# Performance work log

Measured on AMD Instinct MI355X. Metric: run time of the kernel, lower is better.

The kernel has to match this reference:

```python
import jax, jax.numpy as jnp
import numpy as np

HOPS = 3

def setup_inputs() -> dict:
    key = jax.random.key(0)
    ks = jax.random.split(key, 8)
    B, M, S, C, V, D = 16, 200, 32, 2048, 32000, 128
    stories = jax.random.randint(ks[0], (B, M, S), 0, V)
    query = jax.random.randint(ks[1], (B, S), 0, V)
    E = jax.random.randint(ks[2], (B, C, S), 0, V)
    candidates = jax.random.randint(ks[3], (C, S), 0, V)
    # nn.Embedding / nn.Linear weights init: normal(0, 0.1); embedding row 0 zeroed (pad)
    embed_A = (jax.random.normal(ks[4], (V, D), jnp.float32) * 0.1).at[0].set(0.0)
    embed_W = (jax.random.normal(ks[5], (V, D), jnp.float32) * 0.1).at[0].set(0.0)
    H_w = jax.random.normal(ks[6], (D, D), jnp.float32) * 0.1
    H_b = jnp.zeros((D,), jnp.float32)
    return {"stories": stories, "query": query, "E": E, "candidates": candidates,
            "embed_A": embed_A, "embed_W": embed_W, "H_w": H_w, "H_b": H_b}

def reference(stories, query, E, candidates, embed_A, embed_W, H_w, H_b):
    # query embedding, summed over sentence words -> [B, D]
    u = embed_A[query].sum(axis=1)
    # story sentence embeddings summed over words -> [B, M, D]
    # (original recomputes this every hop; value is identical, compute once)
    m = embed_A[stories].sum(axis=2)
    for _ in range(HOPS):
        attn = jax.nn.softmax(jnp.einsum('bmd,bd->bm', m, u), axis=-1)  # [B, M]
        o = jnp.einsum('bm,bmd->bd', attn, m)                            # [B, D]
        u = u @ H_w.T + H_b + o                                          # linear_H(u) + o
    # candidate embeddings: shared candidates table + per-batch mask E, summed over words
    # (embed_W[cand] + embed_W[E]).sum over sentence == sum(embed_W[cand]) + sum(embed_W[E])
    cand_sum = embed_W[candidates].sum(axis=1)[None, :, :] + embed_W[E].sum(axis=2)  # [B, C, D]
    logits = jnp.einsum('bd,bcd->bc', u, cand_sum)  # [B, C]
    return logits
```

## Files before the change

kernel.cpp:

```cpp
#include <hip/hip_runtime.h>

#define B_ 16
#define M_ 200
#define S_ 32
#define C_ 2048
#define V_ 32000
#define D_ 128
#define HOPS_ 3

__global__ void k_embed(const int* __restrict__ stories, const int* __restrict__ query,
                        const float* __restrict__ embA,
                        float* __restrict__ m, float* __restrict__ u0) {
    int lane = threadIdx.x & 31;
    int sent = (blockIdx.x * 256 + threadIdx.x) >> 5;
    if (sent >= B_ * M_ + B_) return;
    const int* idx;
    float* dst;
    if (sent < B_ * M_) { idx = stories + sent * S_; dst = m + sent * D_; }
    else { int b = sent - B_ * M_; idx = query + b * S_; dst = u0 + b * D_; }
    float4 acc = {0.f, 0.f, 0.f, 0.f};
#pragma unroll 8
    for (int s = 0; s < S_; ++s) {
        const float4* row = (const float4*)(embA + (size_t)idx[s] * D_);
        float4 a = row[lane];
        acc.x += a.x; acc.y += a.y; acc.z += a.z; acc.w += a.w;
    }
    ((float4*)dst)[lane] = acc;
}

__global__ void __launch_bounds__(1024) k_hops(
        const float* __restrict__ m, const float* __restrict__ u0,
        const float* __restrict__ Hw, const float* __restrict__ Hb,
        float* __restrict__ uF) {
    const int b = blockIdx.x;
    const int t = threadIdx.x;
    const int lane = t & 63;
    const int wave = t >> 6;

    __shared__ float sm[M_][D_];
    __shared__ float su[D_];
    __shared__ float sattn[M_];
    __shared__ float sred[16 * D_];
    __shared__ float smx, ssum;

    {
        const float4* src = (const float4*)(m + (size_t)b * M_ * D_);
        float4* dst = (float4*)sm;
        for (int j = t; j < M_ * D_ / 4; j += 1024) dst[j] = src[j];
    }
    if (t < D_) su[t] = u0[b * D_ + t];
    __syncthreads();

    for (int hop = 0; hop < HOPS_; ++hop) {
        float2 uu = ((const float2*)su)[lane];
        for (int i = wave; i < M_; i += 16) {
            float2 mv = ((const float2*)sm[i])[lane];
            float p = mv.x * uu.x + mv.y * uu.y;
#pragma unroll
            for (int o = 32; o; o >>= 1) p += __shfl_xor(p, o);
            if (lane == 0) sattn[i] = p;
        }
        __syncthreads();
        if (wave == 0) {
            float mx = -3.0e38f;
            for (int i = lane; i < M_; i += 64) mx = fmaxf(mx, sattn[i]);
#pragma unroll
            for (int o = 32; o; o >>= 1) mx = fmaxf(mx, __shfl_xor(mx, o));
            float sm_ = 0.f;
            for (int i = lane; i < M_; i += 64) sm_ += expf(sattn[i] - mx);
#pragma unroll
            for (int o = 32; o; o >>= 1) sm_ += __shfl_xor(sm_, o);
            if (lane == 0) { smx = mx; ssum = sm_; }
        }
        __syncthreads();
        if (t < M_) sattn[t] = expf(sattn[t] - smx) * (1.f / ssum);
        __syncthreads();
        float2 oacc = {0.f, 0.f};
        for (int i = wave; i < M_; i += 16) {
            float a = sattn[i];
            float2 mv = ((const float2*)sm[i])[lane];
            oacc.x += a * mv.x; oacc.y += a * mv.y;
        }
        ((float2*)sred)[wave * 64 + lane] = oacc;
        __syncthreads();
        int d  = t >> 3;
        int k8 = t & 7;
        float tot = sred[k8 * D_ + d] + sred[(k8 + 8) * D_ + d];
        for (int k = k8; k < D_; k += 8) tot += Hw[d * D_ + k] * su[k];
#pragma unroll
        for (int o = 1; o < 8; o <<= 1) tot += __shfl_xor(tot, o);
        float un = Hb[d] + tot;
        __syncthreads();
        if (k8 == 0) su[d] = un;
        __syncthreads();
    }
    if (t < D_) uF[b * D_ + t] = su[t];
}

__global__ void __launch_bounds__(256) k_pv(
        const float* __restrict__ uF, const float* __restrict__ embW,
        float* __restrict__ P) {
    const int t = threadIdx.x;
    const int gtid = blockIdx.x * 256 + t;
    const int v = gtid >> 2;
    const int q = t & 3;

    __shared__ float4 su4[16 * 36];
    {
#pragma unroll
        for (int it = 0; it < 2; ++it) {
            int f = t + it * 256;
            int b = f >> 5, k = f & 31;
            su4[b * 36 + (k >> 3) * 9 + (k & 7)] = ((const float4*)uF)[f];
        }
    }
    __syncthreads();

    const float4* w = (const float4*)(embW + (size_t)v * D_) + q * 8;
    float acc[16];
#pragma unroll
    for (int b = 0; b < 16; ++b) acc[b] = 0.f;
#pragma unroll
    for (int j = 0; j < 8; ++j) {
        float4 a = w[j];
#pragma unroll
        for (int b = 0; b < 16; ++b) {
            float4 x = su4[b * 36 + q * 9 + j];
            acc[b] += a.x * x.x + a.y * x.y + a.z * x.z + a.w * x.w;
        }
    }
#pragma unroll
    for (int b = 0; b < 16; ++b) {
        acc[b] += __shfl_xor(acc[b], 1);
        acc[b] += __shfl_xor(acc[b], 2);
    }
    float4 o;
    o.x = acc[q * 4 + 0]; o.y = acc[q * 4 + 1];
    o.z = acc[q * 4 + 2]; o.w = acc[q * 4 + 3];
    ((float4*)(P + (size_t)v * B_))[q] = o;
}

__global__ void k_logits(const int* __restrict__ cand, const int* __restrict__ E,
                         const float* __restrict__ P, float* __restrict__ out) {
    int g4 = blockIdx.x * 256 + threadIdx.x;
    int q = g4 & 3;
    int g = g4 >> 2;
    int c = g & (C_ - 1);
    int b = g >> 11;
    const int4* cs = (const int4*)(cand + c * S_ + q * 8);
    const int4* es = (const int4*)(E + (size_t)g * S_ + q * 8);
    float acc = 0.f;
#pragma unroll
    for (int j = 0; j < 2; ++j) {
        int4 wv = cs[j];
        acc += P[wv.x * B_ + b] + P[wv.y * B_ + b] + P[wv.z * B_ + b] + P[wv.w * B_ + b];
        int4 ev = es[j];
        acc += P[ev.x * B_ + b] + P[ev.y * B_ + b] + P[ev.z * B_ + b] + P[ev.w * B_ + b];
    }
    acc += __shfl_xor(acc, 1);
    acc += __shfl_xor(acc, 2);
    if (q == 0) out[g] = acc;
}

extern "C" void kernel_launch(void* const* d_in, const int* in_sizes, int n_in,
                              void* d_out, int out_size, void* d_ws, size_t ws_size,
                              hipStream_t stream) {
    const int*   stories = (const int*)d_in[0];
    const int*   query   = (const int*)d_in[1];
    const int*   E       = (const int*)d_in[2];
    const int*   cand    = (const int*)d_in[3];
    const float* embA    = (const float*)d_in[4];
    const float* embW    = (const float*)d_in[5];
    const float* Hw      = (const float*)d_in[6];
    const float* Hb      = (const float*)d_in[7];
    float* out = (float*)d_out;

    char* ws = (char*)d_ws;
    float* u0 = (float*)ws;
    float* uF = (float*)(ws + 8192);
    float* m  = (float*)(ws + 16384);
    float* P  = (float*)(ws + 16384 + (size_t)B_ * M_ * D_ * 4);

    hipLaunchKernelGGL(k_embed,  dim3((B_ * M_ + B_) * 32 / 256), dim3(256), 0, stream,
                       stories, query, embA, m, u0);
    hipLaunchKernelGGL(k_hops,   dim3(B_), dim3(1024), 0, stream, m, u0, Hw, Hb, uF);
    hipLaunchKernelGGL(k_pv,     dim3(V_ * 4 / 256), dim3(256), 0, stream, uF, embW, P);
    hipLaunchKernelGGL(k_logits, dim3((B_ * C_ * 4) / 256), dim3(256), 0, stream,
                       cand, E, P, out);
}
```

Before: 59.79 us.

## Move query embedding into hops kernel, two vocab rows per thread, split logits gathers

The query embedding sum moves out of the story-embedding kernel into the start of the hops kernel, which removes the u0 buffer and the per-thread branch in k_embed. The vocab projection kernel now has each thread handle two embedding rows, halving the grid and reusing each shared-memory u load for two rows. The logits kernel now uses 8 threads per output, splitting candidate and E gathers across lanes for more memory-level parallelism, at the cost of one extra shuffle step. Doubling the per-thread accumulators in k_pv raises register pressure and may lower occupancy.

After: 63.30 us. +5.9%, slower.

```diff
diff --git a/kernel.cpp b/kernel.cpp
--- a/kernel.cpp
+++ b/kernel.cpp
@@ -8,16 +8,12 @@
 #define D_ 128
 #define HOPS_ 3
 
-__global__ void k_embed(const int* __restrict__ stories, const int* __restrict__ query,
-                        const float* __restrict__ embA,
-                        float* __restrict__ m, float* __restrict__ u0) {
+__global__ void k_embed(const int* __restrict__ stories,
+                        const float* __restrict__ embA, float* __restrict__ m) {
     int lane = threadIdx.x & 31;
     int sent = (blockIdx.x * 256 + threadIdx.x) >> 5;
-    if (sent >= B_ * M_ + B_) return;
-    const int* idx;
-    float* dst;
-    if (sent < B_ * M_) { idx = stories + sent * S_; dst = m + sent * D_; }
-    else { int b = sent - B_ * M_; idx = query + b * S_; dst = u0 + b * D_; }
+    const int* idx = stories + sent * S_;
+    float* dst = m + sent * D_;
     float4 acc = {0.f, 0.f, 0.f, 0.f};
 #pragma unroll 8
     for (int s = 0; s < S_; ++s) {
@@ -29,9 +25,9 @@
 }
 
 __global__ void __launch_bounds__(1024) k_hops(
-        const float* __restrict__ m, const float* __restrict__ u0,
-        const float* __restrict__ Hw, const float* __restrict__ Hb,
-        float* __restrict__ uF) {
+        const float* __restrict__ m, const int* __restrict__ query,
+        const float* __restrict__ embA, const float* __restrict__ Hw,
+        const float* __restrict__ Hb, float* __restrict__ uF) {
     const int b = blockIdx.x;
     const int t = threadIdx.x;
     const int lane = t & 63;
@@ -48,7 +44,12 @@
         float4* dst = (float4*)sm;
         for (int j = t; j < M_ * D_ / 4; j += 1024) dst[j] = src[j];
     }
-    if (t < D_) su[t] = u0[b * D_ + t];
+    if (t < D_) {
+        float a = 0.f;
+#pragma unroll 8
+        for (int s = 0; s < S_; ++s) a += embA[(size_t)query[b * S_ + s] * D_ + t];
+        su[t] = a;
+    }
     __syncthreads();
 
     for (int hop = 0; hop < HOPS_; ++hop) {
@@ -102,8 +103,9 @@
         float* __restrict__ P) {
     const int t = threadIdx.x;
     const int gtid = blockIdx.x * 256 + t;
-    const int v = gtid >> 2;
+    const int p = gtid >> 2;
     const int q = t & 3;
+    const int v0 = p * 2;
 
     __shared__ float4 su4[16 * 36];
     {
@@ -116,49 +118,57 @@
     }
     __syncthreads();
 
-    const float4* w = (const float4*)(embW + (size_t)v * D_) + q * 8;
-    float acc[16];
-#pragma unroll
-    for (int b = 0; b < 16; ++b) acc[b] = 0.f;
+    const float4* w0 = (const float4*)(embW + (size_t)v0 * D_) + q * 8;
+    const float4* w1 = (const float4*)(embW + (size_t)(v0 + 1) * D_) + q * 8;
+    float acc0[16], acc1[16];
+#pragma unroll
+    for (int b = 0; b < 16; ++b) { acc0[b] = 0.f; acc1[b] = 0.f; }
 #pragma unroll
     for (int j = 0; j < 8; ++j) {
-        float4 a = w[j];
+        float4 a0 = w0[j];
+        float4 a1 = w1[j];
 #pragma unroll
         for (int b = 0; b < 16; ++b) {
             float4 x = su4[b * 36 + q * 9 + j];
-            acc[b] += a.x * x.x + a.y * x.y + a.z * x.z + a.w * x.w;
+            acc0[b] += a0.x * x.x + a0.y * x.y + a0.z * x.z + a0.w * x.w;
+            acc1[b] += a1.x * x.x + a1.y * x.y + a1.z * x.z + a1.w * x.w;
         }
     }
 #pragma unroll
     for (int b = 0; b < 16; ++b) {
-        acc[b] += __shfl_xor(acc[b], 1);
-        acc[b] += __shfl_xor(acc[b], 2);
-    }
-    float4 o;
-    o.x = acc[q * 4 + 0]; o.y = acc[q * 4 + 1];
-    o.z = acc[q * 4 + 2]; o.w = acc[q * 4 + 3];
-    ((float4*)(P + (size_t)v * B_))[q] = o;
+        acc0[b] += __shfl_xor(acc0[b], 1);
+        acc0[b] += __shfl_xor(acc0[b], 2);
+        acc1[b] += __shfl_xor(acc1[b], 1);
+        acc1[b] += __shfl_xor(acc1[b], 2);
+    }
+    float4 o0, o1;
+    o0.x = acc0[q * 4 + 0]; o0.y = acc0[q * 4 + 1];
+    o0.z = acc0[q * 4 + 2]; o0.w = acc0[q * 4 + 3];
+    o1.x = acc1[q * 4 + 0]; o1.y = acc1[q * 4 + 1];
+    o1.z = acc1[q * 4 + 2]; o1.w = acc1[q * 4 + 3];
+    ((float4*)(P + (size_t)v0 * B_))[q] = o0;
+    ((float4*)(P + (size_t)(v0 + 1) * B_))[q] = o1;
 }
 
 __global__ void k_logits(const int* __restrict__ cand, const int* __restrict__ E,
                          const float* __restrict__ P, float* __restrict__ out) {
-    int g4 = blockIdx.x * 256 + threadIdx.x;
-    int q = g4 & 3;
-    int g = g4 >> 2;
+    int g8 = blockIdx.x * 256 + threadIdx.x;
+    int q = g8 & 7;
+    int g = g8 >> 3;
     int c = g & (C_ - 1);
     int b = g >> 11;
-    const int4* cs = (const int4*)(cand + c * S_ + q * 8);
-    const int4* es = (const int4*)(E + (size_t)g * S_ + q * 8);
+    const int4* src;
+    if (q < 4) src = (const int4*)(cand + c * S_ + q * 8);
+    else       src = (const int4*)(E + (size_t)g * S_ + (q - 4) * 8);
     float acc = 0.f;
 #pragma unroll
     for (int j = 0; j < 2; ++j) {
-        int4 wv = cs[j];
-        acc += P[wv.x * B_ + b] + P[wv.y * B_ + b] + P[wv.z * B_ + b] + P[wv.w * B_ + b];
-        int4 ev = es[j];
-        acc += P[ev.x * B_ + b] + P[ev.y * B_ + b] + P[ev.z * B_ + b] + P[ev.w * B_ + b];
+        int4 w = src[j];
+        acc += P[w.x * B_ + b] + P[w.y * B_ + b] + P[w.z * B_ + b] + P[w.w * B_ + b];
     }
     acc += __shfl_xor(acc, 1);
     acc += __shfl_xor(acc, 2);
+    acc += __shfl_xor(acc, 4);
     if (q == 0) out[g] = acc;
 }
 
@@ -176,15 +186,15 @@
     float* out = (float*)d_out;
 
     char* ws = (char*)d_ws;
-    float* u0 = (float*)ws;
-    float* uF = (float*)(ws + 8192);
-    float* m  = (float*)(ws + 16384);
-    float* P  = (float*)(ws + 16384 + (size_t)B_ * M_ * D_ * 4);
-
-    hipLaunchKernelGGL(k_embed,  dim3((B_ * M_ + B_) * 32 / 256), dim3(256), 0, stream,
-                       stories, query, embA, m, u0);
-    hipLaunchKernelGGL(k_hops,   dim3(B_), dim3(1024), 0, stream, m, u0, Hw, Hb, uF);
-    hipLaunchKernelGGL(k_pv,     dim3(V_ * 4 / 256), dim3(256), 0, stream, uF, embW, P);
-    hipLaunchKernelGGL(k_logits, dim3((B_ * C_ * 4) / 256), dim3(256), 0, stream,
+    float* uF = (float*)ws;
+    float* m  = (float*)(ws + 8192);
+    float* P  = (float*)(ws + 8192 + (size_t)B_ * M_ * D_ * 4);
+
+    hipLaunchKernelGGL(k_embed,  dim3(B_ * M_ * 32 / 256), dim3(256), 0, stream,
+                       stories, embA, m);
+    hipLaunchKernelGGL(k_hops,   dim3(B_), dim3(1024), 0, stream,
+                       m, query, embA, Hw, Hb, uF);
+    hipLaunchKernelGGL(k_pv,     dim3(V_ * 2 / 256), dim3(256), 0, stream, uF, embW, P);
+    hipLaunchKernelGGL(k_logits, dim3((B_ * C_ * 8) / 256), dim3(256), 0, stream,
                        cand, E, P, out);
 }
```
